# Performance work log

Measured on AMD Instinct MI355X. Metric: run time of the kernel, lower is better.

The kernel has to match this reference:

```python
import jax, jax.numpy as jnp
import numpy as np

N_IN, C, T, E, N_OUT, F = 50000, 64, 8, 800000, 50000, 64


def setup_inputs() -> dict:
    key = jax.random.key(0)
    k0, k1, k2, k3, k4 = jax.random.split(key, 5)
    node_features = jax.random.normal(k0, (N_IN, C), dtype=jnp.float32)
    edge_features = jax.random.normal(k1, (T, E), dtype=jnp.float32)
    idx_out = jax.random.randint(k2, (E,), 0, N_OUT)
    idx_in = jax.random.randint(k3, (E,), 0, N_IN)
    indices = jnp.stack([idx_out, idx_in], axis=1).astype(jnp.int64)  # [E, 2]
    # glorot-ish scale for kernel [T, C, F]
    scale = np.sqrt(2.0 / (C + F)).astype(np.float32)
    kernel = jax.random.normal(k4, (T, C, F), dtype=jnp.float32) * scale
    bias = jnp.zeros((F,), dtype=jnp.float32)
    return {
        "node_features": node_features,
        "edge_features": edge_features,
        "indices": indices,
        "kernel": kernel,
        "bias": bias,
        "out_size": N_OUT,
    }


def reference(node_features, edge_features, indices, kernel, bias, out_size):
    # sparse_conv (combine='unstack'):
    #   out[i] = sum_t ( segment_sum_{e: out(e)=i} ef[t,e] * x[in(e)] ) @ kernel[t] + bias
    gathered = node_features[indices[:, 1]]          # [E, C] irregular gather
    seg_ids = indices[:, 0]
    n_terms = kernel.shape[0]                        # small fixed structural dim
    out = jnp.zeros((out_size, kernel.shape[2]), dtype=node_features.dtype)
    for t in range(n_terms):
        weighted = edge_features[t][:, None] * gathered            # [E, C]
        agg = jax.ops.segment_sum(weighted, seg_ids, num_segments=out_size)  # [No, C]
        out = out + agg @ kernel[t]                                # [No, F]
    return out + bias
```

## Files before the change

### kernel.cpp

```cpp
#include <hip/hip_runtime.h>

constexpr int N_IN  = 50000;
constexpr int C     = 64;
constexpr int T     = 8;
constexpr int E     = 800000;
constexpr int N_OUT = 50000;
constexpr int F     = 64;

constexpr int CHUNK  = 2048;
constexpr int NCHUNK = (E + CHUNK - 1) / CHUNK;
constexpr int NBIN_S = (N_OUT + 255) / 256;
constexpr int CAP    = 5120;

constexpr size_t OFF_NFBF  = 0;
constexpr size_t OFF_KT    = 6400000;
constexpr size_t OFF_BCUR  = OFF_KT + 65536;
constexpr size_t OFF_START = OFF_BCUR + 1024;
constexpr size_t OFF_ENT   = OFF_START + 200064;
constexpr size_t OFF_ENT2  = OFF_ENT + 4014080;
constexpr size_t OFF_BINW  = OFF_ENT2 + 3200000;
static_assert(OFF_ENT % 16 == 0 && OFF_BINW % 16 == 0, "alignment");

typedef __attribute__((ext_vector_type(8))) short short8;
typedef __attribute__((ext_vector_type(4))) float f32x4;

__device__ inline unsigned short f2bf(float x) {
    unsigned int u = __float_as_uint(x);
    unsigned int r = (u + 0x7FFFu + ((u >> 16) & 1u)) >> 16;
    return (unsigned short)r;
}
__device__ inline float bf2f(unsigned short u) {
    return __uint_as_float(((unsigned int)u) << 16);
}

constexpr int BS_BLOCKS = NCHUNK;
constexpr int NF_BLOCKS = (N_IN * C / 4 + 511) / 512;
constexpr int KT_BLOCKS = T * C * F / 512;

__global__ __launch_bounds__(512) void fused_prep_kernel(
        const float* __restrict__ nf,
        const float* __restrict__ Kmat,
        const float* __restrict__ ef,
        const int* __restrict__ idx,
        unsigned short* __restrict__ nf_bf,
        unsigned short* __restrict__ K_T,
        int* __restrict__ bincur,
        unsigned* __restrict__ ent,
        float* __restrict__ binw) {
    __shared__ int hist[NBIN_S];
    __shared__ int scb[NBIN_S];
    __shared__ int cur[NBIN_S];
    __shared__ int gdel[NBIN_S];
    __shared__ int sscan[256];
    __shared__ unsigned sgu[CHUNK];
    __shared__ unsigned short sge[CHUNK];
    __shared__ unsigned char sgb[CHUNK];

    const int b   = blockIdx.x;
    const int tid = threadIdx.x;

    if (b < BS_BLOCKS) {
        for (int i = tid; i < NBIN_S; i += 512) hist[i] = 0;
        __syncthreads();
        const int e0 = b * CHUNK;
        const int n  = min(CHUNK, E - e0);
        for (int i = tid; i < n; i += 512)
            atomicAdd(&hist[((const int2*)idx)[e0 + i].x >> 8], 1);
        __syncthreads();
        if (tid < 256) sscan[tid] = (tid < NBIN_S) ? hist[tid] : 0;
        __syncthreads();
        for (int off = 1; off < 256; off <<= 1) {
            int x = 0;
            if (tid < 256 && tid >= off) x = sscan[tid - off];
            __syncthreads();
            if (tid < 256 && tid >= off) sscan[tid] += x;
            __syncthreads();
        }
        if (tid < NBIN_S) {
            int e = sscan[tid] - hist[tid];
            scb[tid] = e;
            cur[tid] = e;
        }
        __syncthreads();
        for (int bb = tid; bb < NBIN_S; bb += 512) {
            int c = hist[bb];
            if (c > 0)
                gdel[bb] = bb * CAP + atomicAdd(&bincur[bb], c) - scb[bb];
        }
        __syncthreads();
        for (int i = tid; i < n; i += 512) {
            int2 oi = ((const int2*)idx)[e0 + i];
            int bin = oi.x >> 8;
            int r = atomicAdd(&cur[bin], 1);
            sgu[r] = ((unsigned)(oi.x & 255) << 16) | (unsigned)oi.y;
            sge[r] = (unsigned short)i;
            sgb[r] = (unsigned char)bin;
        }
        __syncthreads();
        for (int i = tid; i < n; i += 512) {
            int bin  = sgb[i];
            int pos  = gdel[bin] + i;
            if (pos < (bin + 1) * CAP) {
                int eoff = sge[i];
                float w[8];
#pragma unroll
                for (int t = 0; t < T; ++t) w[t] = ef[(size_t)t * E + e0 + eoff];
                ent[pos] = sgu[i];
                float4* dst = (float4*)(binw + (size_t)pos * 8);
                dst[0] = make_float4(w[0], w[1], w[2], w[3]);
                dst[1] = make_float4(w[4], w[5], w[6], w[7]);
            }
        }
    } else if (b < BS_BLOCKS + NF_BLOCKS) {
        int i = (b - BS_BLOCKS) * 512 + tid;
        if (i < N_IN * C / 4) {
            float4 v = ((const float4*)nf)[i];
            unsigned int u0 = (unsigned int)f2bf(v.x) | ((unsigned int)f2bf(v.y) << 16);
            unsigned int u1 = (unsigned int)f2bf(v.z) | ((unsigned int)f2bf(v.w) << 16);
            ((uint2*)nf_bf)[i] = make_uint2(u0, u1);
        }
    } else {
        int k = (b - BS_BLOCKS - NF_BLOCKS) * 512 + tid;
        int f = k & 63;
        int c = (k >> 6) & 63;
        int t = k >> 12;
        K_T[f * 512 + t * 64 + c] = f2bf(Kmat[k]);
    }
}

__global__ __launch_bounds__(512) void permfix_kernel(const int* __restrict__ bincur,
                                                      const unsigned* __restrict__ ent,
                                                      int* __restrict__ start_g,
                                                      unsigned* __restrict__ ent2) {
    __shared__ int sh[768];
    const int tid = threadIdx.x;
    const int b   = blockIdx.x;

    sh[tid] = (tid < b) ? bincur[tid] : 0;
    __syncthreads();
#pragma unroll
    for (int off = 256; off >= 1; off >>= 1) {
        if (tid < off) sh[tid] += sh[tid + off];
        __syncthreads();
    }
    const int base2 = sh[0];
    const int cnt   = min(bincur[b], CAP);
    const int W0p   = b * CAP;
    __syncthreads();

    int* hist = sh;
    int* sc   = sh + 256;
    int* cur  = sh + 512;

    if (tid < 256) hist[tid] = 0;
    __syncthreads();
    for (int i = W0p + tid; i < W0p + cnt; i += 512)
        atomicAdd(&hist[ent[i] >> 16], 1);
    __syncthreads();

    if (tid < 256) sc[tid] = hist[tid];
    __syncthreads();
    for (int off = 1; off < 256; off <<= 1) {
        int x = 0;
        if (tid < 256 && tid >= off) x = sc[tid - off];
        __syncthreads();
        if (tid < 256 && tid >= off) sc[tid] += x;
        __syncthreads();
    }
    if (tid < 256) {
        int s = base2 + sc[tid] - hist[tid];
        int g = b * 256 + tid;
        if (g < N_OUT) start_g[g] = s;
        cur[tid] = s;
    }
    if (b == NBIN_S - 1 && tid == 0) start_g[N_OUT] = E;
    __syncthreads();

    for (int i = W0p + tid; i < W0p + cnt; i += 512) {
        unsigned u = ent[i];
        int loc = (int)(u >> 16);
        int pos = atomicAdd(&cur[loc], 1);
        ent2[pos] = ((unsigned)(i - W0p) << 16) | (u & 0xFFFFu);
    }
}

__global__ __launch_bounds__(256) void aggregate_kernel(const unsigned short* __restrict__ nf_bf,
                                                        const unsigned short* __restrict__ K_T,
                                                        const int* __restrict__ start,
                                                        const unsigned* __restrict__ ent2,
                                                        const float* __restrict__ binw,
                                                        const float* __restrict__ bias,
                                                        float* __restrict__ out) {
    __shared__ unsigned short A_lds[16][520];

    constexpr int NWG = N_OUT / 16;
    constexpr int Q = NWG / 8, R = NWG % 8;
    const int xc = blockIdx.x & 7;
    const int sl = blockIdx.x >> 3;
    const int orig = (xc < R ? xc * (Q + 1) : R * (Q + 1) + (xc - R) * Q) + sl;

    const int wave = threadIdx.x >> 6;
    const int lane = threadIdx.x & 63;
    const int node_base = orig * 16;
    const int Wbase = (orig >> 4) * CAP;

    for (int q = 0; q < 4; ++q) {
        const int m = wave * 4 + q;
        const int o = node_base + m;
        const int s0 = __builtin_amdgcn_readfirstlane(start[o]);
        const int s1 = __builtin_amdgcn_readfirstlane(start[o + 1]);

        float acc[8] = {0.f, 0.f, 0.f, 0.f, 0.f, 0.f, 0.f, 0.f};

        for (int base = s0; base < s1; base += 64) {
            const int cnt = min(64, s1 - base);
            int vv = (base + lane < s1) ? (int)ent2[base + lane] : 0;

            int j = 0;
            for (; j + 4 <= cnt; j += 4) {
                const int v0 = __builtin_amdgcn_readlane(vv, j + 0);
                const int v1 = __builtin_amdgcn_readlane(vv, j + 1);
                const int v2 = __builtin_amdgcn_readlane(vv, j + 2);
                const int v3 = __builtin_amdgcn_readlane(vv, j + 3);
                float x0 = bf2f(nf_bf[(size_t)(v0 & 0xFFFF) * 64 + lane]);
                float x1 = bf2f(nf_bf[(size_t)(v1 & 0xFFFF) * 64 + lane]);
                float x2 = bf2f(nf_bf[(size_t)(v2 & 0xFFFF) * 64 + lane]);
                float x3 = bf2f(nf_bf[(size_t)(v3 & 0xFFFF) * 64 + lane]);
                const float* w0 = binw + (size_t)(Wbase + (((unsigned)v0) >> 16)) * 8;
                const float* w1 = binw + (size_t)(Wbase + (((unsigned)v1) >> 16)) * 8;
                const float* w2 = binw + (size_t)(Wbase + (((unsigned)v2) >> 16)) * 8;
                const float* w3 = binw + (size_t)(Wbase + (((unsigned)v3) >> 16)) * 8;
#pragma unroll
                for (int t = 0; t < T; ++t) {
                    acc[t] += w0[t] * x0;
                    acc[t] += w1[t] * x1;
                    acc[t] += w2[t] * x2;
                    acc[t] += w3[t] * x3;
                }
            }
            for (; j < cnt; ++j) {
                const int v0 = __builtin_amdgcn_readlane(vv, j);
                float x0 = bf2f(nf_bf[(size_t)(v0 & 0xFFFF) * 64 + lane]);
                const float* w0 = binw + (size_t)(Wbase + (((unsigned)v0) >> 16)) * 8;
#pragma unroll
                for (int t = 0; t < T; ++t) acc[t] += w0[t] * x0;
            }
        }

#pragma unroll
        for (int t = 0; t < T; ++t) A_lds[m][t * 64 + lane] = f2bf(acc[t]);
    }
    __syncthreads();

    const int mrow = lane & 15;
    const int kb   = lane >> 4;
    const int fcol = wave * 16 + mrow;

    f32x4 acc4 = {0.f, 0.f, 0.f, 0.f};
#pragma unroll
    for (int s = 0; s < 16; ++s) {
        const int k0 = s * 32 + kb * 8;
        short8 a = *(const short8*)&A_lds[mrow][k0];
        short8 b = *(const short8*)(K_T + (size_t)fcol * 512 + k0);
        acc4 = __builtin_amdgcn_mfma_f32_16x16x32_bf16(a, b, acc4, 0, 0, 0);
    }

    const float bv = bias[fcol];
#pragma unroll
    for (int r = 0; r < 4; ++r) {
        const int m = kb * 4 + r;
        out[(size_t)(node_base + m) * F + fcol] = acc4[r] + bv;
    }
}

extern "C" void kernel_launch(void* const* d_in, const int* in_sizes, int n_in,
                              void* d_out, int out_size, void* d_ws, size_t ws_size,
                              hipStream_t stream) {
    const float* nf   = (const float*)d_in[0];
    const float* ef   = (const float*)d_in[1];
    const int*   idx  = (const int*)d_in[2];
    const float* Kmat = (const float*)d_in[3];
    const float* bias = (const float*)d_in[4];
    float*       out  = (float*)d_out;

    char* ws = (char*)d_ws;
    unsigned short* nf_bf  = (unsigned short*)(ws + OFF_NFBF);
    unsigned short* K_T    = (unsigned short*)(ws + OFF_KT);
    int*            bincur = (int*)(ws + OFF_BCUR);
    int*            start  = (int*)(ws + OFF_START);
    unsigned*       ent    = (unsigned*)(ws + OFF_ENT);
    unsigned*       ent2   = (unsigned*)(ws + OFF_ENT2);
    float*          binw   = (float*)(ws + OFF_BINW);

    hipMemsetAsync(bincur, 0, NBIN_S * sizeof(int), stream);
    fused_prep_kernel<<<BS_BLOCKS + NF_BLOCKS + KT_BLOCKS, 512, 0, stream>>>(
        nf, Kmat, ef, idx, nf_bf, K_T, bincur, ent, binw);
    permfix_kernel<<<NBIN_S, 512, 0, stream>>>(bincur, ent, start, ent2);
    aggregate_kernel<<<N_OUT / 16, 256, 0, stream>>>(
        nf_bf, K_T, start, ent2, binw, bias, out);
}
```

Baseline: 181.8 us.

## Fuse per-node sorting into aggregate kernel, dropping permfix pass

Removes the separate permfix kernel that built global per-node start offsets and a reordered edge list. Each aggregate workgroup now scans its whole 256-node bin, filters the entries for its own 16 nodes, and counting-sorts them in LDS before the gather/accumulate. This saves a kernel launch and the global write and read of start/ent2. In exchange every bin's entries are read 16 times (once per workgroup), and each block can hold at most 512 edges; any overflow is silently dropped.

```diff
diff --git a/kernel.cpp b/kernel.cpp
--- a/kernel.cpp
+++ b/kernel.cpp
@@ -12,13 +12,11 @@
 constexpr int NBIN_S = (N_OUT + 255) / 256;
 constexpr int CAP    = 5120;
 
-constexpr size_t OFF_NFBF  = 0;
-constexpr size_t OFF_KT    = 6400000;
-constexpr size_t OFF_BCUR  = OFF_KT + 65536;
-constexpr size_t OFF_START = OFF_BCUR + 1024;
-constexpr size_t OFF_ENT   = OFF_START + 200064;
-constexpr size_t OFF_ENT2  = OFF_ENT + 4014080;
-constexpr size_t OFF_BINW  = OFF_ENT2 + 3200000;
+constexpr size_t OFF_NFBF = 0;
+constexpr size_t OFF_KT   = 6400000;
+constexpr size_t OFF_BCUR = OFF_KT + 65536;
+constexpr size_t OFF_ENT  = OFF_BCUR + 1024;
+constexpr size_t OFF_BINW = OFF_ENT + 4014080;
 static_assert(OFF_ENT % 16 == 0 && OFF_BINW % 16 == 0, "alignment");
 
 typedef __attribute__((ext_vector_type(8))) short short8;
@@ -128,70 +126,22 @@
     }
 }
 
-__global__ __launch_bounds__(512) void permfix_kernel(const int* __restrict__ bincur,
-                                                      const unsigned* __restrict__ ent,
-                                                      int* __restrict__ start_g,
-                                                      unsigned* __restrict__ ent2) {
-    __shared__ int sh[768];
-    const int tid = threadIdx.x;
-    const int b   = blockIdx.x;
-
-    sh[tid] = (tid < b) ? bincur[tid] : 0;
-    __syncthreads();
-#pragma unroll
-    for (int off = 256; off >= 1; off >>= 1) {
-        if (tid < off) sh[tid] += sh[tid + off];
-        __syncthreads();
-    }
-    const int base2 = sh[0];
-    const int cnt   = min(bincur[b], CAP);
-    const int W0p   = b * CAP;
-    __syncthreads();
-
-    int* hist = sh;
-    int* sc   = sh + 256;
-    int* cur  = sh + 512;
-
-    if (tid < 256) hist[tid] = 0;
-    __syncthreads();
-    for (int i = W0p + tid; i < W0p + cnt; i += 512)
-        atomicAdd(&hist[ent[i] >> 16], 1);
-    __syncthreads();
-
-    if (tid < 256) sc[tid] = hist[tid];
-    __syncthreads();
-    for (int off = 1; off < 256; off <<= 1) {
-        int x = 0;
-        if (tid < 256 && tid >= off) x = sc[tid - off];
-        __syncthreads();
-        if (tid < 256 && tid >= off) sc[tid] += x;
-        __syncthreads();
-    }
-    if (tid < 256) {
-        int s = base2 + sc[tid] - hist[tid];
-        int g = b * 256 + tid;
-        if (g < N_OUT) start_g[g] = s;
-        cur[tid] = s;
-    }
-    if (b == NBIN_S - 1 && tid == 0) start_g[N_OUT] = E;
-    __syncthreads();
-
-    for (int i = W0p + tid; i < W0p + cnt; i += 512) {
-        unsigned u = ent[i];
-        int loc = (int)(u >> 16);
-        int pos = atomicAdd(&cur[loc], 1);
-        ent2[pos] = ((unsigned)(i - W0p) << 16) | (u & 0xFFFFu);
-    }
-}
-
-__global__ __launch_bounds__(256) void aggregate_kernel(const unsigned short* __restrict__ nf_bf,
-                                                        const unsigned short* __restrict__ K_T,
-                                                        const int* __restrict__ start,
-                                                        const unsigned* __restrict__ ent2,
-                                                        const float* __restrict__ binw,
-                                                        const float* __restrict__ bias,
-                                                        float* __restrict__ out) {
+__global__ __launch_bounds__(256) void aggregate_kernel(
+        const unsigned short* __restrict__ nf_bf,
+        const unsigned short* __restrict__ K_T,
+        const int* __restrict__ bincur,
+        const unsigned* __restrict__ ent,
+        const float* __restrict__ binw,
+        const float* __restrict__ bias,
+        float* __restrict__ out) {
     __shared__ unsigned short A_lds[16][520];
+    __shared__ unsigned tmp[512];
+    __shared__ unsigned sent[512];
+    __shared__ unsigned char tmpl[512];
+    __shared__ int h16[16];
+    __shared__ int sst[17];
+    __shared__ int cur16[16];
+    __shared__ int cnt0;
 
     constexpr int NWG = N_OUT / 16;
     constexpr int Q = NWG / 8, R = NWG % 8;
@@ -199,56 +149,85 @@
     const int sl = blockIdx.x >> 3;
     const int orig = (xc < R ? xc * (Q + 1) : R * (Q + 1) + (xc - R) * Q) + sl;
 
-    const int wave = threadIdx.x >> 6;
-    const int lane = threadIdx.x & 63;
+    const int tid  = threadIdx.x;
+    const int wave = tid >> 6;
+    const int lane = tid & 63;
     const int node_base = orig * 16;
-    const int Wbase = (orig >> 4) * CAP;
+    const int bin  = orig >> 4;
+    const int lo   = (orig & 15) << 4;
+    const int W0p  = bin * CAP;
+    const int cnt  = min(bincur[bin], CAP);
+
+    if (tid == 0) cnt0 = 0;
+    if (tid < 16) h16[tid] = 0;
+    __syncthreads();
+    for (int rel = tid; rel < cnt; rel += 256) {
+        unsigned u = ent[W0p + rel];
+        int d = (int)(u >> 16) - lo;
+        if ((unsigned)d < 16u) {
+            int p = atomicAdd(&cnt0, 1);
+            if (p < 512) {
+                tmp[p]  = ((unsigned)rel << 16) | (u & 0xFFFFu);
+                tmpl[p] = (unsigned char)d;
+                atomicAdd(&h16[d], 1);
+            }
+        }
+    }
+    __syncthreads();
+    const int m0 = min(cnt0, 512);
+    if (tid == 0) {
+        int s = 0;
+        for (int k = 0; k < 16; ++k) { sst[k] = s; s += h16[k]; }
+        sst[16] = s;
+    }
+    __syncthreads();
+    if (tid < 16) cur16[tid] = sst[tid];
+    __syncthreads();
+    for (int i = tid; i < m0; i += 256) {
+        int p = atomicAdd(&cur16[tmpl[i]], 1);
+        sent[p] = tmp[i];
+    }
+    __syncthreads();
 
     for (int q = 0; q < 4; ++q) {
-        const int m = wave * 4 + q;
-        const int o = node_base + m;
-        const int s0 = __builtin_amdgcn_readfirstlane(start[o]);
-        const int s1 = __builtin_amdgcn_readfirstlane(start[o + 1]);
+        const int nl = wave * 4 + q;
+        const int s0 = sst[nl];
+        const int s1 = sst[nl + 1];
 
         float acc[8] = {0.f, 0.f, 0.f, 0.f, 0.f, 0.f, 0.f, 0.f};
 
-        for (int base = s0; base < s1; base += 64) {
-            const int cnt = min(64, s1 - base);
-            int vv = (base + lane < s1) ? (int)ent2[base + lane] : 0;
-
-            int j = 0;
-            for (; j + 4 <= cnt; j += 4) {
-                const int v0 = __builtin_amdgcn_readlane(vv, j + 0);
-                const int v1 = __builtin_amdgcn_readlane(vv, j + 1);
-                const int v2 = __builtin_amdgcn_readlane(vv, j + 2);
-                const int v3 = __builtin_amdgcn_readlane(vv, j + 3);
-                float x0 = bf2f(nf_bf[(size_t)(v0 & 0xFFFF) * 64 + lane]);
-                float x1 = bf2f(nf_bf[(size_t)(v1 & 0xFFFF) * 64 + lane]);
-                float x2 = bf2f(nf_bf[(size_t)(v2 & 0xFFFF) * 64 + lane]);
-                float x3 = bf2f(nf_bf[(size_t)(v3 & 0xFFFF) * 64 + lane]);
-                const float* w0 = binw + (size_t)(Wbase + (((unsigned)v0) >> 16)) * 8;
-                const float* w1 = binw + (size_t)(Wbase + (((unsigned)v1) >> 16)) * 8;
-                const float* w2 = binw + (size_t)(Wbase + (((unsigned)v2) >> 16)) * 8;
-                const float* w3 = binw + (size_t)(Wbase + (((unsigned)v3) >> 16)) * 8;
-#pragma unroll
-                for (int t = 0; t < T; ++t) {
-                    acc[t] += w0[t] * x0;
-                    acc[t] += w1[t] * x1;
-                    acc[t] += w2[t] * x2;
-                    acc[t] += w3[t] * x3;
-                }
+        int j = s0;
+        for (; j + 4 <= s1; j += 4) {
+            const int u0 = __builtin_amdgcn_readfirstlane((int)sent[j + 0]);
+            const int u1 = __builtin_amdgcn_readfirstlane((int)sent[j + 1]);
+            const int u2 = __builtin_amdgcn_readfirstlane((int)sent[j + 2]);
+            const int u3 = __builtin_amdgcn_readfirstlane((int)sent[j + 3]);
+            float x0 = bf2f(nf_bf[(size_t)(u0 & 0xFFFF) * 64 + lane]);
+            float x1 = bf2f(nf_bf[(size_t)(u1 & 0xFFFF) * 64 + lane]);
+            float x2 = bf2f(nf_bf[(size_t)(u2 & 0xFFFF) * 64 + lane]);
+            float x3 = bf2f(nf_bf[(size_t)(u3 & 0xFFFF) * 64 + lane]);
+            const float* w0 = binw + (size_t)(W0p + (((unsigned)u0) >> 16)) * 8;
+            const float* w1 = binw + (size_t)(W0p + (((unsigned)u1) >> 16)) * 8;
+            const float* w2 = binw + (size_t)(W0p + (((unsigned)u2) >> 16)) * 8;
+            const float* w3 = binw + (size_t)(W0p + (((unsigned)u3) >> 16)) * 8;
+#pragma unroll
+            for (int t = 0; t < T; ++t) {
+                acc[t] += w0[t] * x0;
+                acc[t] += w1[t] * x1;
+                acc[t] += w2[t] * x2;
+                acc[t] += w3[t] * x3;
             }
-            for (; j < cnt; ++j) {
-                const int v0 = __builtin_amdgcn_readlane(vv, j);
-                float x0 = bf2f(nf_bf[(size_t)(v0 & 0xFFFF) * 64 + lane]);
-                const float* w0 = binw + (size_t)(Wbase + (((unsigned)v0) >> 16)) * 8;
-#pragma unroll
-                for (int t = 0; t < T; ++t) acc[t] += w0[t] * x0;
-            }
-        }
-
-#pragma unroll
-        for (int t = 0; t < T; ++t) A_lds[m][t * 64 + lane] = f2bf(acc[t]);
+        }
+        for (; j < s1; ++j) {
+            const int u0 = __builtin_amdgcn_readfirstlane((int)sent[j]);
+            float x0 = bf2f(nf_bf[(size_t)(u0 & 0xFFFF) * 64 + lane]);
+            const float* w0 = binw + (size_t)(W0p + (((unsigned)u0) >> 16)) * 8;
+#pragma unroll
+            for (int t = 0; t < T; ++t) acc[t] += w0[t] * x0;
+        }
+
+#pragma unroll
+        for (int t = 0; t < T; ++t) A_lds[nl][t * 64 + lane] = f2bf(acc[t]);
     }
     __syncthreads();
 
@@ -261,8 +240,8 @@
     for (int s = 0; s < 16; ++s) {
         const int k0 = s * 32 + kb * 8;
         short8 a = *(const short8*)&A_lds[mrow][k0];
-        short8 b = *(const short8*)(K_T + (size_t)fcol * 512 + k0);
-        acc4 = __builtin_amdgcn_mfma_f32_16x16x32_bf16(a, b, acc4, 0, 0, 0);
+        short8 bm = *(const short8*)(K_T + (size_t)fcol * 512 + k0);
+        acc4 = __builtin_amdgcn_mfma_f32_16x16x32_bf16(a, bm, acc4, 0, 0, 0);
     }
 
     const float bv = bias[fcol];
@@ -287,15 +266,12 @@
     unsigned short* nf_bf  = (unsigned short*)(ws + OFF_NFBF);
     unsigned short* K_T    = (unsigned short*)(ws + OFF_KT);
     int*            bincur = (int*)(ws + OFF_BCUR);
-    int*            start  = (int*)(ws + OFF_START);
     unsigned*       ent    = (unsigned*)(ws + OFF_ENT);
-    unsigned*       ent2   = (unsigned*)(ws + OFF_ENT2);
     float*          binw   = (float*)(ws + OFF_BINW);
 
     hipMemsetAsync(bincur, 0, NBIN_S * sizeof(int), stream);
     fused_prep_kernel<<<BS_BLOCKS + NF_BLOCKS + KT_BLOCKS, 512, 0, stream>>>(
         nf, Kmat, ef, idx, nf_bf, K_T, bincur, ent, binw);
-    permfix_kernel<<<NBIN_S, 512, 0, stream>>>(bincur, ent, start, ent2);
     aggregate_kernel<<<N_OUT / 16, 256, 0, stream>>>(
-        nf_bf, K_T, start, ent2, binw, bias, out);
-}
+        nf_bf, K_T, bincur, ent, binw, bias, out);
+}
```

Result: no change. 182.8 us (+0.6%).
